# Optimization experiments

Hardware: AMD Instinct MI355X
Metric: run time of the kernel (lower is better)

Reference implementation:

```python
import jax, jax.numpy as jnp
import numpy as np

B, T, E, D = 8, 2048, 2048, 256  # batch, seq (== max_seq_len), embed_size, block_size

def setup_inputs() -> dict:
    key = jax.random.key(0)
    kx, kq, kk, kv = jax.random.split(key, 4)
    x = jax.random.normal(kx, (B, T, E), dtype=jnp.float32)
    s = 1.0 / np.sqrt(E)
    Wq = jax.random.normal(kq, (E, D), dtype=jnp.float32) * s
    Wk = jax.random.normal(kk, (E, D), dtype=jnp.float32) * s
    Wv = jax.random.normal(kv, (E, D), dtype=jnp.float32) * s
    return {"x": x, "Wq": Wq, "Wk": Wk, "Wv": Wv}

def reference(x, Wq, Wk, Wv):
    # q,k,v: [B, T, D]
    q = jnp.einsum('bte,ed->btd', x, Wq)
    k = jnp.einsum('bte,ed->btd', x, Wk)
    v = jnp.einsum('bte,ed->btd', x, Wv)
    scores = jnp.einsum('bqd,bkd->bqk', q, k)  # [B, T, T]
    causal = jnp.tril(jnp.ones((T, T), dtype=bool))
    scores = jnp.where(causal, scores, -jnp.inf)
    inv_sqrt_d = 1.0 / np.sqrt(D).astype(np.float32)
    # Original divides by sqrt(D) twice: once before softmax, once inside -> net 1/D scale
    scores = scores * inv_sqrt_d
    attn = jax.nn.softmax(scores * inv_sqrt_d, axis=-1)
    z = jnp.einsum('bqk,bkd->bqd', attn, v)
    return z
```

## Files before the change

### kernel.cpp

```cpp
#include <hip/hip_runtime.h>
#include <hip/hip_bf16.h>

typedef unsigned short u16;
typedef unsigned int u32;
typedef __attribute__((ext_vector_type(8))) __bf16 bf16x8;
typedef __attribute__((ext_vector_type(4))) float f32x4;
typedef __attribute__((ext_vector_type(16))) float f32x16;
typedef __attribute__((ext_vector_type(2))) unsigned u32x2;
typedef __attribute__((ext_vector_type(4))) unsigned short u16x4;

__device__ __forceinline__ u16 f2bf(float f) {
  u32 u = __builtin_bit_cast(u32, f);
  return (u16)((u + 0x7fffu + ((u >> 16) & 1u)) >> 16);
}
__device__ __forceinline__ float bf2f(u16 h) {
  u32 u = ((u32)h) << 16;
  return __builtin_bit_cast(float, u);
}
__device__ __forceinline__ u32 pk2(float lo, float hi) {
  union { __bf16 b[2]; u32 u; } r;
  r.b[0] = (__bf16)lo; r.b[1] = (__bf16)hi;
  return r.u;
}

__device__ __forceinline__ void pl32pair(u32& a, u32& b) {
#if __has_builtin(__builtin_amdgcn_permlane32_swap)
  u32x2 r = __builtin_amdgcn_permlane32_swap(a, b, 0, 0);
  a = r.x; b = r.y;
#else
  int hi = (int)((threadIdx.x & 63) >> 5);
  u32 as = __shfl_xor(a, 32), bs = __shfl_xor(b, 32);
  u32 na = hi ? bs : a;
  u32 nb = hi ? b : as;
  a = na; b = nb;
#endif
}
__device__ __forceinline__ float red_max32(float x) {
  u32 a = __builtin_bit_cast(u32, x), b = __builtin_bit_cast(u32, x);
  pl32pair(a, b);
  return fmaxf(__builtin_bit_cast(float, a), __builtin_bit_cast(float, b));
}
__device__ __forceinline__ float red_sum32(float x) {
  u32 a = __builtin_bit_cast(u32, x), b = __builtin_bit_cast(u32, x);
  pl32pair(a, b);
  return __builtin_bit_cast(float, a) + __builtin_bit_cast(float, b);
}

__global__ __launch_bounds__(256) void cast_x_kernel(const float* __restrict__ x,
                                                     u16* __restrict__ xb) {
  size_t i = ((size_t)blockIdx.x * 256 + threadIdx.x) * 8;
  float4 a = *(const float4*)(x + i);
  float4 b = *(const float4*)(x + i + 4);
  union { u16 h[8]; uint4 v; } o;
  o.h[0] = f2bf(a.x); o.h[1] = f2bf(a.y); o.h[2] = f2bf(a.z); o.h[3] = f2bf(a.w);
  o.h[4] = f2bf(b.x); o.h[5] = f2bf(b.y); o.h[6] = f2bf(b.z); o.h[7] = f2bf(b.w);
  *(uint4*)(xb + i) = o.v;
}

__global__ void cast_w_kernel(const float* __restrict__ Wq, const float* __restrict__ Wk,
                              const float* __restrict__ Wv, u16* __restrict__ wbt) {
  __shared__ float tile[32][33];
  int e0 = blockIdx.x * 32, d0 = blockIdx.y * 32, w = blockIdx.z;
  const float* W = (w == 0) ? Wq : ((w == 1) ? Wk : Wv);
  int x = threadIdx.x, y = threadIdx.y;
#pragma unroll
  for (int j = 0; j < 4; j++)
    tile[y + j * 8][x] = W[(size_t)(e0 + y + j * 8) * 256 + d0 + x];
  __syncthreads();
#pragma unroll
  for (int j = 0; j < 4; j++)
    wbt[(size_t)(w * 256 + d0 + y + j * 8) * 2048 + e0 + x] = f2bf(tile[x][y + j * 8]);
}

__global__ __launch_bounds__(256, 2) void gemm_kernel(const u16* __restrict__ A,
                                                      const u16* __restrict__ Bt,
                                                      u16* __restrict__ qbuf,
                                                      u16* __restrict__ kfrag,
                                                      u16* __restrict__ vfrag) {
  __shared__ __align__(16) u16 As[3][4096];
  __shared__ __align__(16) u16 Bs[3][6144];

  int tid = threadIdx.x;
  int w = tid >> 6, l = tid & 63;
  int lr = l & 15, lg = l >> 4;
  int wm = w >> 1, wn = w & 1;

  int bid = blockIdx.x;
  int xcd = bid & 7;
  int idx = bid >> 3;
  int rowb = xcd * 16 + (idx >> 2);
  int colb = idx & 3;
  int row0 = rowb * 128, col0 = colb * 192;

  int garow = w * 16 + (l >> 2);
  int scol = ((l & 3) * 8) ^ (((l >> 3) & 3) * 8);
  const u16* ga = A + (size_t)(row0 + garow) * 2048 + scol;
  const u16* gb = Bt + (size_t)(col0 + garow) * 2048 + scol;

  f32x4 acc[4][6];
#pragma unroll
  for (int m = 0; m < 4; m++)
#pragma unroll
    for (int n = 0; n < 6; n++) acc[m][n] = (f32x4){0.f, 0.f, 0.f, 0.f};

  int rcol = (lg * 8) ^ (((lr >> 1) & 3) * 8);

#define STAGE_A3(ts, bi)                                                               \
  {                                                                                    \
    _Pragma("unroll") for (int c = 0; c < 2; c++)                                      \
        __builtin_amdgcn_global_load_lds(                                              \
            (const __attribute__((address_space(1))) void*)(ga + (size_t)c * 64 * 2048 + (ts) * 32), \
            (__attribute__((address_space(3))) void*)&As[bi][(c * 64 + w * 16) * 32], 16, 0, 0); \
  }
#define STAGE_B3(ts, bi)                                                               \
  {                                                                                    \
    _Pragma("unroll") for (int c = 0; c < 3; c++)                                      \
        __builtin_amdgcn_global_load_lds(                                              \
            (const __attribute__((address_space(1))) void*)(gb + (size_t)c * 64 * 2048 + (ts) * 32), \
            (__attribute__((address_space(3))) void*)&Bs[bi][(c * 64 + w * 16) * 32], 16, 0, 0); \
  }

  STAGE_A3(0, 0); STAGE_B3(0, 0);
  STAGE_A3(1, 1); STAGE_B3(1, 1);
  asm volatile("s_waitcnt vmcnt(5)" ::: "memory");
  __builtin_amdgcn_s_barrier();

  int bi = 0, bp = 2;
  for (int t = 0; t < 64; t++) {
    int ts = (t + 2 <= 63) ? (t + 2) : 63;
    const u16* asb = As[bi];
    const u16* bsb = Bs[bi];

    bf16x8 bfr[6], af0, af1;
#pragma unroll
    for (int n = 0; n < 6; n++)
      bfr[n] = *(const bf16x8*)&bsb[(wn * 96 + n * 16 + lr) * 32 + rcol];
    af0 = *(const bf16x8*)&asb[(wm * 64 + 0 * 16 + lr) * 32 + rcol];
    af1 = *(const bf16x8*)&asb[(wm * 64 + 1 * 16 + lr) * 32 + rcol];
    STAGE_A3(ts, bp);
    __builtin_amdgcn_s_barrier();
    asm volatile("s_waitcnt lgkmcnt(0)" ::: "memory");
    __builtin_amdgcn_sched_barrier(0);
    __builtin_amdgcn_s_setprio(1);
#pragma unroll
    for (int n = 0; n < 6; n++) {
      acc[0][n] = __builtin_amdgcn_mfma_f32_16x16x32_bf16(af0, bfr[n], acc[0][n], 0, 0, 0);
      acc[1][n] = __builtin_amdgcn_mfma_f32_16x16x32_bf16(af1, bfr[n], acc[1][n], 0, 0, 0);
    }
    __builtin_amdgcn_s_setprio(0);
    __builtin_amdgcn_s_barrier();

    bf16x8 af2, af3;
    af2 = *(const bf16x8*)&asb[(wm * 64 + 2 * 16 + lr) * 32 + rcol];
    af3 = *(const bf16x8*)&asb[(wm * 64 + 3 * 16 + lr) * 32 + rcol];
    STAGE_B3(ts, bp);
    __builtin_amdgcn_s_barrier();
    asm volatile("s_waitcnt lgkmcnt(0)" ::: "memory");
    __builtin_amdgcn_sched_barrier(0);
    __builtin_amdgcn_s_setprio(1);
#pragma unroll
    for (int n = 0; n < 6; n++) {
      acc[2][n] = __builtin_amdgcn_mfma_f32_16x16x32_bf16(af2, bfr[n], acc[2][n], 0, 0, 0);
      acc[3][n] = __builtin_amdgcn_mfma_f32_16x16x32_bf16(af3, bfr[n], acc[3][n], 0, 0, 0);
    }
    __builtin_amdgcn_s_setprio(0);
    asm volatile("s_waitcnt vmcnt(5)" ::: "memory");
    __builtin_amdgcn_s_barrier();

    bi = (bi == 2) ? 0 : bi + 1;
    bp = (bp == 2) ? 0 : bp + 1;
  }
#undef STAGE_A3
#undef STAGE_B3

  int crow = row0 + wm * 64;
#pragma unroll
  for (int m = 0; m < 4; m++) {
    int t0 = crow + m * 16 + lg * 4;
    int bb = t0 >> 11, tm0 = t0 & 2047;
#pragma unroll
    for (int n = 0; n < 6; n++) {
      int cb = col0 + wn * 96 + n * 16;
      int c = cb + lr;
      if (cb < 256) {
#pragma unroll
        for (int i = 0; i < 4; i++)
          qbuf[(size_t)(t0 + i) * 256 + c] = f2bf(acc[m][n][i]);
      } else if (cb < 512) {
        int kc = c - 256;
        int kvb = tm0 >> 5;
        int t16 = kc >> 4;
        int lhalf = (kc >> 3) & 1;
        int jj = kc & 7;
        size_t base = ((size_t)((bb * 64 + kvb) * 16 + t16) * 64 + lhalf * 32) * 8 + jj;
#pragma unroll
        for (int i = 0; i < 4; i++)
          kfrag[base + (size_t)((tm0 + i) & 31) * 8] = f2bf(acc[m][n][i]);
      } else {
        int vc = c - 512;
        int kvb = tm0 >> 5;
        int ch = (tm0 >> 4) & 1;
        int lhalf = (tm0 >> 3) & 1;
        int jj = tm0 & 7;
        int dblk = vc >> 5;
        int lane = (vc & 31) + lhalf * 32;
        size_t base = ((size_t)(((bb * 64 + kvb) * 2 + ch) * 8 + dblk) * 64 + lane) * 8 + jj;
        u16x4 pk = {f2bf(acc[m][n][0]), f2bf(acc[m][n][1]),
                    f2bf(acc[m][n][2]), f2bf(acc[m][n][3])};
        *(u16x4*)(vfrag + base) = pk;
      }
    }
  }
}

__global__ __launch_bounds__(512, 2) void attn_kernel(const u16* __restrict__ qbuf,
                                                      const u16* __restrict__ kfrag,
                                                      const u16* __restrict__ vfrag,
                                                      float* __restrict__ out) {
  __shared__ __align__(16) u16 qlds[16 * 512];
  __shared__ __align__(16) u16 klds[4 * 16 * 512];
  __shared__ float facc[32][264];
  __shared__ float sm[4][32];
  __shared__ float sl[4][32];

  int tid = threadIdx.x;
  int w = tid >> 6, l = tid & 63;
  int ql = l & 31, hi = l >> 5;
  int stream = w & 3, dhalf = w >> 2;
  int bid = blockIdx.x;
  int b = bid & 7;
  int p = bid >> 3;

  for (int tile = 0; tile < 2; tile++) {
    int jt = tile ? p : (63 - p);
    int q0 = jt * 32;

    if (tile) __syncthreads();
#pragma unroll
    for (int c = 0; c < 2; c++) {
      int m = c * 512 + tid;
      int t16 = m >> 6, ll = m & 63;
      const u16* src = qbuf + (size_t)(b * 2048 + q0 + (ll & 31)) * 256 + t16 * 16 + (ll >> 5) * 8;
      union { u16 h[8]; bf16x8 v; } in, ov;
      in.v = *(const bf16x8*)src;
#pragma unroll
      for (int j = 0; j < 8; j++) ov.h[j] = f2bf(bf2f(in.h[j]) * (1.0f / 256.0f));
      *(bf16x8*)&qlds[(t16 * 64 + ll) * 8] = ov.v;
    }
    __syncthreads();

    f32x16 o[4];
#pragma unroll
    for (int d = 0; d < 4; d++)
#pragma unroll
      for (int r = 0; r < 16; r++) o[d][r] = 0.f;
    float mreg = -__builtin_inff(), ell = 0.f;

    int nround = (jt >> 2) + 1;
    for (int rr = 0; rr < nround; rr++) {
      int jb = rr * 4 + stream;
      bool act = (jb <= jt);

      if (w < 4 && act) {
#pragma unroll
        for (int t = 0; t < 16; t++)
          __builtin_amdgcn_global_load_lds(
              (const __attribute__((address_space(1))) void*)(
                  kfrag + ((size_t)((b * 64 + jb) * 16 + t) * 64 + l) * 8),
              (__attribute__((address_space(3))) void*)&klds[(stream * 16 + t) * 512],
              16, 0, 0);
      }
      if (w < 4) asm volatile("s_waitcnt vmcnt(0)" ::: "memory");
      __syncthreads();

      if (act) {
        const u16* vb = vfrag + ((size_t)(b * 64 + jb) * 16 * 64 + l) * 8;
        bf16x8 ve0[4], ve1[4];
#pragma unroll
        for (int dd = 0; dd < 4; dd++) {
          ve0[dd] = *(const bf16x8*)(vb + (dhalf * 4 + dd) * 512);
          ve1[dd] = *(const bf16x8*)(vb + (8 + dhalf * 4 + dd) * 512);
        }

        const u16* kl = &klds[(stream * 16 * 64 + l) * 8];
        f32x16 sA, sB;
#pragma unroll
        for (int r = 0; r < 16; r++) { sA[r] = 0.f; sB[r] = 0.f; }
#pragma unroll
        for (int g = 0; g < 4; g++) {
          bf16x8 k0 = *(const bf16x8*)(kl + (g * 4 + 0) * 512);
          bf16x8 k1 = *(const bf16x8*)(kl + (g * 4 + 1) * 512);
          bf16x8 k2 = *(const bf16x8*)(kl + (g * 4 + 2) * 512);
          bf16x8 k3 = *(const bf16x8*)(kl + (g * 4 + 3) * 512);
          bf16x8 q0f = *(const bf16x8*)&qlds[((g * 4 + 0) * 64 + l) * 8];
          bf16x8 q1f = *(const bf16x8*)&qlds[((g * 4 + 1) * 64 + l) * 8];
          bf16x8 q2f = *(const bf16x8*)&qlds[((g * 4 + 2) * 64 + l) * 8];
          bf16x8 q3f = *(const bf16x8*)&qlds[((g * 4 + 3) * 64 + l) * 8];
          sA = __builtin_amdgcn_mfma_f32_32x32x16_bf16(k0, q0f, sA, 0, 0, 0);
          sB = __builtin_amdgcn_mfma_f32_32x32x16_bf16(k1, q1f, sB, 0, 0, 0);
          sA = __builtin_amdgcn_mfma_f32_32x32x16_bf16(k2, q2f, sA, 0, 0, 0);
          sB = __builtin_amdgcn_mfma_f32_32x32x16_bf16(k3, q3f, sB, 0, 0, 0);
        }

        float s[16];
#pragma unroll
        for (int r = 0; r < 16; r++) s[r] = sA[r] + sB[r];

        if (jb == jt) {
#pragma unroll
          for (int r = 0; r < 16; r++) {
            int kv = (r & 3) + 8 * (r >> 2) + 4 * hi;
            if (kv > ql) s[r] = -__builtin_inff();
          }
        }

        float mx = s[0];
#pragma unroll
        for (int r = 1; r < 16; r++) mx = fmaxf(mx, s[r]);
        mx = red_max32(mx);
        if (__any(mx > mreg + 8.f)) {
          float mnew = fmaxf(mreg, mx);
          float sf = __expf(mreg - mnew);
          mreg = mnew;
          ell *= sf;
#pragma unroll
          for (int d = 0; d < 4; d++)
#pragma unroll
            for (int r = 0; r < 16; r++) o[d][r] *= sf;
        }
        float pr[16], ps = 0.f;
#pragma unroll
        for (int r = 0; r < 16; r++) { pr[r] = __expf(s[r] - mreg); ps += pr[r]; }
        ell += red_sum32(ps);

        u32 wv[8];
#pragma unroll
        for (int i = 0; i < 8; i++) wv[i] = pk2(pr[2 * i], pr[2 * i + 1]);
        pl32pair(wv[0], wv[2]); pl32pair(wv[1], wv[3]);
        pl32pair(wv[4], wv[6]); pl32pair(wv[5], wv[7]);
        union { u32 u[4]; bf16x8 v; } B0, B1;
        B0.u[0] = wv[0]; B0.u[1] = wv[1]; B0.u[2] = wv[2]; B0.u[3] = wv[3];
        B1.u[0] = wv[4]; B1.u[1] = wv[5]; B1.u[2] = wv[6]; B1.u[3] = wv[7];

#pragma unroll
        for (int dd = 0; dd < 4; dd++) {
          o[dd] = __builtin_amdgcn_mfma_f32_32x32x16_bf16(ve0[dd], B0.v, o[dd], 0, 0, 0);
          o[dd] = __builtin_amdgcn_mfma_f32_32x32x16_bf16(ve1[dd], B1.v, o[dd], 0, 0, 0);
        }
      }
      __syncthreads();
    }

    if (w < 4 && l < 32) { sm[w][l] = mreg; sl[w][l] = ell; }
    __syncthreads();

    float M = fmaxf(fmaxf(sm[0][ql], sm[1][ql]), fmaxf(sm[2][ql], sm[3][ql]));
    float alpha = __expf(mreg - M);

#pragma unroll
    for (int ph = 0; ph < 4; ph++) {
      if (stream == ph) {
#pragma unroll
        for (int dd = 0; dd < 4; dd++)
#pragma unroll
          for (int rq = 0; rq < 4; rq++) {
            int base = (dhalf * 4 + dd) * 32 + 8 * rq + 4 * hi;
            f32x4 v;
#pragma unroll
            for (int i = 0; i < 4; i++) v[i] = alpha * o[dd][rq * 4 + i];
            float* fp = &facc[ql][base];
            if (ph == 0) *(f32x4*)fp = v;
            else {
              f32x4 old = *(const f32x4*)fp;
              *(f32x4*)fp = old + v;
            }
          }
      }
      __syncthreads();
    }

    int r = tid >> 4, lt = tid & 15;
    float Mr = fmaxf(fmaxf(sm[0][r], sm[1][r]), fmaxf(sm[2][r], sm[3][r]));
    float denom = 0.f;
#pragma unroll
    for (int ww = 0; ww < 4; ww++) denom += __expf(sm[ww][r] - Mr) * sl[ww][r];
    float inv = 1.0f / denom;
    float* orow = out + (size_t)(b * 2048 + q0 + r) * 256;
#pragma unroll
    for (int j = 0; j < 4; j++) {
      int c = (lt + j * 16) * 4;
      f32x4 v = *(const f32x4*)&facc[r][c];
      v[0] *= inv; v[1] *= inv; v[2] *= inv; v[3] *= inv;
      *(f32x4*)&orow[c] = v;
    }
  }
}

extern "C" void kernel_launch(void* const* d_in, const int* in_sizes, int n_in,
                              void* d_out, int out_size, void* d_ws, size_t ws_size,
                              hipStream_t stream) {
  (void)in_sizes; (void)n_in; (void)out_size; (void)ws_size;
  const float* x = (const float*)d_in[0];
  const float* Wq = (const float*)d_in[1];
  const float* Wk = (const float*)d_in[2];
  const float* Wv = (const float*)d_in[3];
  float* out = (float*)d_out;

  char* ws = (char*)d_ws;
  u16* xb    = (u16*)(ws);
  u16* wbt   = (u16*)(ws + 67108864);
  u16* qbuf  = (u16*)(ws + 70254592);
  u16* kfrag = (u16*)(ws + 78643200);
  u16* vfrag = (u16*)(ws + 87031808);

  cast_x_kernel<<<16384, 256, 0, stream>>>(x, xb);
  cast_w_kernel<<<dim3(64, 8, 3), dim3(32, 8), 0, stream>>>(Wq, Wk, Wv, wbt);
  gemm_kernel<<<512, 256, 0, stream>>>(xb, wbt, qbuf, kfrag, vfrag);
  attn_kernel<<<256, 512, 0, stream>>>(qbuf, kfrag, vfrag, out);
}
```

Measured before the change: 139.1 us.

## Fuse fp32-to-bf16 cast of x into the projection GEMM A-tile staging

Removes the separate cast_x kernel that wrote a bf16 copy of x. The GEMM now loads fp32 x into registers, converts to bf16, and writes the swizzled A tile to LDS itself, with a register stage one iteration ahead. This saves a full read and write pass over x (128MB fp32 read plus 64MB bf16 write). The cost is double the global read bytes for A inside the GEMM, higher register pressure, and VALU conversion work in the main loop. The wait counts change to match.

```diff
diff --git a/kernel.cpp b/kernel.cpp
--- a/kernel.cpp
+++ b/kernel.cpp
@@ -46,17 +46,6 @@
   return __builtin_bit_cast(float, a) + __builtin_bit_cast(float, b);
 }
 
-__global__ __launch_bounds__(256) void cast_x_kernel(const float* __restrict__ x,
-                                                     u16* __restrict__ xb) {
-  size_t i = ((size_t)blockIdx.x * 256 + threadIdx.x) * 8;
-  float4 a = *(const float4*)(x + i);
-  float4 b = *(const float4*)(x + i + 4);
-  union { u16 h[8]; uint4 v; } o;
-  o.h[0] = f2bf(a.x); o.h[1] = f2bf(a.y); o.h[2] = f2bf(a.z); o.h[3] = f2bf(a.w);
-  o.h[4] = f2bf(b.x); o.h[5] = f2bf(b.y); o.h[6] = f2bf(b.z); o.h[7] = f2bf(b.w);
-  *(uint4*)(xb + i) = o.v;
-}
-
 __global__ void cast_w_kernel(const float* __restrict__ Wq, const float* __restrict__ Wk,
                               const float* __restrict__ Wv, u16* __restrict__ wbt) {
   __shared__ float tile[32][33];
@@ -72,7 +61,7 @@
     wbt[(size_t)(w * 256 + d0 + y + j * 8) * 2048 + e0 + x] = f2bf(tile[x][y + j * 8]);
 }
 
-__global__ __launch_bounds__(256, 2) void gemm_kernel(const u16* __restrict__ A,
+__global__ __launch_bounds__(256, 2) void gemm_kernel(const float* __restrict__ X,
                                                       const u16* __restrict__ Bt,
                                                       u16* __restrict__ qbuf,
                                                       u16* __restrict__ kfrag,
@@ -92,9 +81,14 @@
   int colb = idx & 3;
   int row0 = rowb * 128, col0 = colb * 192;
 
+  int arow = w * 16 + (l >> 2);
+  int achunk = l & 3;
+  int aswz = achunk ^ ((l >> 3) & 3);
+  const float* gax = X + (size_t)(row0 + arow) * 2048 + achunk * 8;
+  float4 areg[2][2];
+
   int garow = w * 16 + (l >> 2);
   int scol = ((l & 3) * 8) ^ (((l >> 3) & 3) * 8);
-  const u16* ga = A + (size_t)(row0 + garow) * 2048 + scol;
   const u16* gb = Bt + (size_t)(col0 + garow) * 2048 + scol;
 
   f32x4 acc[4][6];
@@ -105,27 +99,43 @@
 
   int rcol = (lg * 8) ^ (((lr >> 1) & 3) * 8);
 
-#define STAGE_A3(ts, bi)                                                               \
-  {                                                                                    \
-    _Pragma("unroll") for (int c = 0; c < 2; c++)                                      \
-        __builtin_amdgcn_global_load_lds(                                              \
-            (const __attribute__((address_space(1))) void*)(ga + (size_t)c * 64 * 2048 + (ts) * 32), \
-            (__attribute__((address_space(3))) void*)&As[bi][(c * 64 + w * 16) * 32], 16, 0, 0); \
-  }
-#define STAGE_B3(ts, bi)                                                               \
-  {                                                                                    \
-    _Pragma("unroll") for (int c = 0; c < 3; c++)                                      \
-        __builtin_amdgcn_global_load_lds(                                              \
+#define LOAD_A(ts)                                                        \
+  {                                                                       \
+    _Pragma("unroll") for (int c = 0; c < 2; c++) {                       \
+      const float* p = gax + (size_t)c * 64 * 2048 + (ts) * 32;           \
+      areg[c][0] = *(const float4*)p;                                     \
+      areg[c][1] = *(const float4*)(p + 4);                               \
+    }                                                                     \
+  }
+#define WRITE_A(bi_)                                                      \
+  {                                                                       \
+    _Pragma("unroll") for (int c = 0; c < 2; c++) {                       \
+      union { u16 h[8]; uint4 v; } oa;                                    \
+      oa.h[0] = f2bf(areg[c][0].x); oa.h[1] = f2bf(areg[c][0].y);         \
+      oa.h[2] = f2bf(areg[c][0].z); oa.h[3] = f2bf(areg[c][0].w);         \
+      oa.h[4] = f2bf(areg[c][1].x); oa.h[5] = f2bf(areg[c][1].y);         \
+      oa.h[6] = f2bf(areg[c][1].z); oa.h[7] = f2bf(areg[c][1].w);         \
+      *(uint4*)&As[bi_][(c * 64 + arow) * 32 + aswz * 8] = oa.v;          \
+    }                                                                     \
+  }
+#define STAGE_B3(ts, bi_)                                                 \
+  {                                                                       \
+    _Pragma("unroll") for (int c = 0; c < 3; c++)                         \
+        __builtin_amdgcn_global_load_lds(                                 \
             (const __attribute__((address_space(1))) void*)(gb + (size_t)c * 64 * 2048 + (ts) * 32), \
-            (__attribute__((address_space(3))) void*)&Bs[bi][(c * 64 + w * 16) * 32], 16, 0, 0); \
-  }
-
-  STAGE_A3(0, 0); STAGE_B3(0, 0);
-  STAGE_A3(1, 1); STAGE_B3(1, 1);
-  asm volatile("s_waitcnt vmcnt(5)" ::: "memory");
+            (__attribute__((address_space(3))) void*)&Bs[bi_][(c * 64 + w * 16) * 32], 16, 0, 0); \
+  }
+
+  LOAD_A(0);
+  WRITE_A(0);
+  LOAD_A(1);
+  STAGE_B3(0, 0);
+  STAGE_B3(1, 1);
+  asm volatile("s_waitcnt vmcnt(3)" ::: "memory");
+  asm volatile("s_waitcnt lgkmcnt(0)" ::: "memory");
   __builtin_amdgcn_s_barrier();
 
-  int bi = 0, bp = 2;
+  int bi = 0, bn = 1, bp = 2;
   for (int t = 0; t < 64; t++) {
     int ts = (t + 2 <= 63) ? (t + 2) : 63;
     const u16* asb = As[bi];
@@ -137,7 +147,8 @@
       bfr[n] = *(const bf16x8*)&bsb[(wn * 96 + n * 16 + lr) * 32 + rcol];
     af0 = *(const bf16x8*)&asb[(wm * 64 + 0 * 16 + lr) * 32 + rcol];
     af1 = *(const bf16x8*)&asb[(wm * 64 + 1 * 16 + lr) * 32 + rcol];
-    STAGE_A3(ts, bp);
+    WRITE_A(bn);
+    LOAD_A(ts);
     __builtin_amdgcn_s_barrier();
     asm volatile("s_waitcnt lgkmcnt(0)" ::: "memory");
     __builtin_amdgcn_sched_barrier(0);
@@ -164,13 +175,15 @@
       acc[3][n] = __builtin_amdgcn_mfma_f32_16x16x32_bf16(af3, bfr[n], acc[3][n], 0, 0, 0);
     }
     __builtin_amdgcn_s_setprio(0);
-    asm volatile("s_waitcnt vmcnt(5)" ::: "memory");
+    asm volatile("s_waitcnt vmcnt(7)" ::: "memory");
     __builtin_amdgcn_s_barrier();
 
     bi = (bi == 2) ? 0 : bi + 1;
+    bn = (bn == 2) ? 0 : bn + 1;
     bp = (bp == 2) ? 0 : bp + 1;
   }
-#undef STAGE_A3
+#undef LOAD_A
+#undef WRITE_A
 #undef STAGE_B3
 
   int crow = row0 + wm * 64;
@@ -407,14 +420,12 @@
   float* out = (float*)d_out;
 
   char* ws = (char*)d_ws;
-  u16* xb    = (u16*)(ws);
   u16* wbt   = (u16*)(ws + 67108864);
   u16* qbuf  = (u16*)(ws + 70254592);
   u16* kfrag = (u16*)(ws + 78643200);
   u16* vfrag = (u16*)(ws + 87031808);
 
-  cast_x_kernel<<<16384, 256, 0, stream>>>(x, xb);
   cast_w_kernel<<<dim3(64, 8, 3), dim3(32, 8), 0, stream>>>(Wq, Wk, Wv, wbt);
-  gemm_kernel<<<512, 256, 0, stream>>>(xb, wbt, qbuf, kfrag, vfrag);
+  gemm_kernel<<<512, 256, 0, stream>>>(x, wbt, qbuf, kfrag, vfrag);
   attn_kernel<<<256, 512, 0, stream>>>(qbuf, kfrag, vfrag, out);
 }
```

Measured after the change: 123.0 us. -11.6%, faster.
